# Performance work log

Measured on AMD Instinct MI355X. Metric: run time of the kernel, lower is better.

The kernel has to match this reference:

```python
import jax, jax.numpy as jnp
import numpy as np
from jax import lax

B, S, H = 1, 2048, 1024
NH, NKV, HD = 16, 4, 64        # heads, kv heads, head_dim = H // NH
I = 3584                        # intermediate size
E, TOPK = 8, 2                  # experts, top-k routing
EPS = 1e-5
THETA = 1e6


def setup_inputs() -> dict:
    key = jax.random.key(0)
    ks = jax.random.split(key, 12)
    sc = 0.02
    return {
        "hidden_states": jax.random.normal(ks[0], (B, S, H), jnp.float32),
        "position_ids": jnp.broadcast_to(jnp.arange(S, dtype=jnp.int32), (B, S)),
        "wq": jax.random.normal(ks[1], (H, NH * HD), jnp.float32) * sc,
        "wk": jax.random.normal(ks[2], (H, NKV * HD), jnp.float32) * sc,
        "wv": jax.random.normal(ks[3], (H, NKV * HD), jnp.float32) * sc,
        "wo": jax.random.normal(ks[4], (NH * HD, H), jnp.float32) * sc,
        "input_norm_w": jnp.ones((H,), jnp.float32),
        "post_norm_w": jnp.ones((H,), jnp.float32),
        "gate_w": jax.random.normal(ks[5], (H, E), jnp.float32) * sc,
        "w1": jax.random.normal(ks[6], (E, H, I), jnp.float32) * sc,
        "w3": jax.random.normal(ks[7], (E, H, I), jnp.float32) * sc,
        "w2": jax.random.normal(ks[8], (E, I, H), jnp.float32) * sc,
    }


def _rmsnorm(x, w):
    var = jnp.mean(jnp.square(x), axis=-1, keepdims=True)
    return x * lax.rsqrt(var + EPS) * w


def _rope(q, k, position_ids):
    # q: [B,S,NH,HD], k: [B,S,NKV,HD]
    inv_freq = 1.0 / (THETA ** (jnp.arange(0, HD, 2, dtype=jnp.float32) / HD))
    freqs = position_ids.astype(jnp.float32)[..., None] * inv_freq  # [B,S,HD/2]
    emb = jnp.concatenate([freqs, freqs], axis=-1)                  # [B,S,HD]
    cos = jnp.cos(emb)[:, :, None, :]
    sin = jnp.sin(emb)[:, :, None, :]

    def rot_half(x):
        x1, x2 = jnp.split(x, 2, axis=-1)
        return jnp.concatenate([-x2, x1], axis=-1)

    return q * cos + rot_half(q) * sin, k * cos + rot_half(k) * sin


def _attention(x, position_ids, wq, wk, wv, wo):
    b, s, _ = x.shape
    q = (x @ wq).reshape(b, s, NH, HD)
    k = (x @ wk).reshape(b, s, NKV, HD)
    v = (x @ wv).reshape(b, s, NKV, HD)
    q, k = _rope(q, k, position_ids)
    groups = NH // NKV
    k = jnp.repeat(k, groups, axis=2)  # [B,S,NH,HD]
    v = jnp.repeat(v, groups, axis=2)
    scale = HD ** -0.5
    scores = jnp.einsum("bqhd,bkhd->bhqk", q, k) * scale
    causal = jnp.tril(jnp.ones((s, s), dtype=bool))
    scores = jnp.where(causal[None, None], scores, jnp.finfo(scores.dtype).min)
    probs = jax.nn.softmax(scores, axis=-1)
    out = jnp.einsum("bhqk,bkhd->bqhd", probs, v).reshape(b, s, NH * HD)
    return out @ wo


def _moe(x, gate_w, w1, w3, w2):
    b, s, h = x.shape
    xt = x.reshape(b * s, h)
    logits = xt @ gate_w                      # [T,E]
    probs = jax.nn.softmax(logits, axis=-1)
    top_w, top_i = lax.top_k(probs, TOPK)     # [T,K]
    top_w = top_w / jnp.sum(top_w, axis=-1, keepdims=True)
    out = jnp.zeros_like(xt)
    for e in range(E):
        we = jnp.sum(jnp.where(top_i == e, top_w, 0.0), axis=-1)   # [T]
        h_e = jax.nn.silu(xt @ w1[e]) * (xt @ w3[e])               # [T,I]
        out = out + we[:, None] * (h_e @ w2[e])
    return out.reshape(b, s, h), logits


def reference(hidden_states, position_ids, wq, wk, wv, wo,
              input_norm_w, post_norm_w, gate_w, w1, w3, w2):
    # MixtralDecoderLayer: norm -> GQA attn -> residual -> norm -> MoE -> residual
    attn_out = _attention(_rmsnorm(hidden_states, input_norm_w),
                          position_ids, wq, wk, wv, wo)
    h = hidden_states + attn_out
    moe_out, _router_logits = _moe(_rmsnorm(h, post_norm_w), gate_w, w1, w3, w2)
    return h + moe_out
```

## Files before the change

kernel.cpp:

```cpp
#include <hip/hip_runtime.h>
#include <math.h>


typedef unsigned short u16;
typedef unsigned int u32;
typedef __attribute__((ext_vector_type(8))) short s16x8;
typedef __attribute__((ext_vector_type(8))) _Float16 f16x8;
typedef __attribute__((ext_vector_type(4))) float f32x4;

#define S_LEN 2048
#define HDIM  1024
#define NHEAD 16
#define NKVH  4
#define HD    64
#define ISZ   3584
#define NEXP  8
#define NSLOT 4096
#define EPS_F 1e-5f
#define NEG_INF -1e30f
#define LOG2E 1.44269504f

__device__ __forceinline__ float bf2f(u16 u) {
    union { u32 i; float f; } c; c.i = ((u32)u) << 16; return c.f;
}
__device__ __forceinline__ u16 f2bf(float f) {
    union { float f; u32 i; } c; c.f = f;
    u32 r = (c.i + 0x7fffu + ((c.i >> 16) & 1u)) >> 16;
    return (u16)r;
}
__device__ __forceinline__ u16 f2h_bits(float f) {
    union { _Float16 h; u16 u; } c; c.h = (_Float16)f; return c.u;
}
__device__ __forceinline__ void async16(const u16* g, u16* l) {
    __builtin_amdgcn_global_load_lds(
        (const __attribute__((address_space(1))) void*)g,
        (__attribute__((address_space(3))) void*)l, 16, 0, 0);
}

__global__ void k_zero_ints(int* __restrict__ p, int n) {
    int i = blockIdx.x * blockDim.x + threadIdx.x;
    if (i < n) p[i] = 0;
}

__global__ __launch_bounds__(256)
void k_rmsnorm_bf(const float* __restrict__ x, const float* __restrict__ w,
                  u16* __restrict__ out) {
    int t = blockIdx.x;
    int tid = threadIdx.x;
    float4 v = ((const float4*)(x + (size_t)t * HDIM))[tid];
    float ss = v.x * v.x + v.y * v.y + v.z * v.z + v.w * v.w;
#pragma unroll
    for (int off = 32; off >= 1; off >>= 1) ss += __shfl_xor(ss, off, 64);
    __shared__ float red[4];
    if ((tid & 63) == 0) red[tid >> 6] = ss;
    __syncthreads();
    float tot = red[0] + red[1] + red[2] + red[3];
    float rstd = rsqrtf(tot * (1.0f / HDIM) + EPS_F);
    float4 wv = ((const float4*)w)[tid];
    uint2 pk;
    pk.x = (u32)f2bf(v.x * rstd * wv.x) | ((u32)f2bf(v.y * rstd * wv.y) << 16);
    pk.y = (u32)f2bf(v.z * rstd * wv.z) | ((u32)f2bf(v.w * rstd * wv.w) << 16);
    ((uint2*)(out + (size_t)t * HDIM))[tid] = pk;
}

__global__ __launch_bounds__(256)
void k_cvt_t(const float* __restrict__ src, u16* __restrict__ dst,
             int R, int C, long long srcZ, long long dstZ) {
    const int z = blockIdx.z;
    src += (size_t)z * srcZ;
    dst += (size_t)z * dstZ;
    const int lane = threadIdx.x & 63, w = threadIdx.x >> 6;
    const int c = blockIdx.x * 64 + lane;
    const int r0 = blockIdx.y * 128 + w * 32;
    float v[32];
#pragma unroll
    for (int i = 0; i < 32; i++) v[i] = src[(size_t)(r0 + i) * C + c];
#pragma unroll
    for (int g = 0; g < 4; g++) {
        uint4 pk;
        pk.x = (u32)f2bf(v[g * 8 + 0]) | ((u32)f2bf(v[g * 8 + 1]) << 16);
        pk.y = (u32)f2bf(v[g * 8 + 2]) | ((u32)f2bf(v[g * 8 + 3]) << 16);
        pk.z = (u32)f2bf(v[g * 8 + 4]) | ((u32)f2bf(v[g * 8 + 5]) << 16);
        pk.w = (u32)f2bf(v[g * 8 + 6]) | ((u32)f2bf(v[g * 8 + 7]) << 16);
        *(uint4*)(&dst[(size_t)c * R + r0 + g * 8]) = pk;
    }
}

__device__ __forceinline__ void gemm128_loop(
    const u16* __restrict__ A, const u16* __restrict__ Bt, int K,
    int rowA0, int rowAmax, int n0, u16* lds, f32x4 acc[4][4]) {
    const int tid = threadIdx.x;
    const int lane = tid & 63, wid = tid >> 6;
    const int sr = lane >> 2, sc = lane & 3;
    const int ln = lane & 15, q = lane >> 4;
    const int wm = wid >> 1, wn = wid & 1;
    for (int k0 = 0; k0 < K; k0 += 32) {
        __syncthreads();
#pragma unroll
        for (int t = 0; t < 2; t++) {
            int row = wid * 32 + t * 16 + sr;
            int ck = (sc ^ (row & 3)) << 3;
            int ra = rowA0 + row;
            if (ra > rowAmax) ra = rowAmax;
            u16* ldsA = lds + (size_t)(wid * 32 + t * 16) * 32;
            u16* ldsB = ldsA + 4096;
            async16(A + (size_t)ra * K + k0 + ck, ldsA);
            async16(Bt + (size_t)(n0 + row) * K + k0 + ck, ldsB);
        }
        __syncthreads();
        s16x8 af[4], bfv[4];
#pragma unroll
        for (int i = 0; i < 4; i++) {
            int ar = wm * 64 + i * 16 + ln;
            af[i] = *(const s16x8*)(lds + ar * 32 + ((q ^ (ar & 3)) << 3));
            int br = wn * 64 + i * 16 + ln;
            bfv[i] = *(const s16x8*)(lds + 4096 + br * 32 + ((q ^ (br & 3)) << 3));
        }
#pragma unroll
        for (int i = 0; i < 4; i++)
#pragma unroll
            for (int j = 0; j < 4; j++)
                acc[i][j] = __builtin_amdgcn_mfma_f32_16x16x32_bf16(
                    af[i], bfv[j], acc[i][j], 0, 0, 0);
    }
}

__global__ __launch_bounds__(256, 2)
void k_gemm_bt(const u16* __restrict__ A, const u16* __restrict__ Bt,
               int M, int N, int K, int mode,
               float* __restrict__ F0, float* __restrict__ F1,
               const float* __restrict__ RES, u16* __restrict__ O16) {
    __shared__ u16 lds[8192];
    const int m0 = blockIdx.y * 128, n0 = blockIdx.x * 128;
    f32x4 acc[4][4];
#pragma unroll
    for (int i = 0; i < 4; i++)
#pragma unroll
        for (int j = 0; j < 4; j++) acc[i][j] = (f32x4){0.f, 0.f, 0.f, 0.f};
    gemm128_loop(A, Bt, K, m0, M - 1, n0, lds, acc);
    const int lane = threadIdx.x & 63, wid = threadIdx.x >> 6;
    const int ln = lane & 15, q = lane >> 4, wm = wid >> 1, wn = wid & 1;
#pragma unroll
    for (int i = 0; i < 4; i++) {
#pragma unroll
        for (int r = 0; r < 4; r++) {
            int m = m0 + wm * 64 + i * 16 + q * 4 + r;
#pragma unroll
            for (int j = 0; j < 4; j++) {
                int n = n0 + wn * 64 + j * 16 + ln;
                float v = acc[i][j][r];
                if (mode == 0) {
                    F0[(size_t)m * N + n] = v;
                } else if (mode == 1) {
                    O16[(size_t)m * N + n] = f2bf(v);
                } else if (mode == 2) {
                    F0[(size_t)m * N + n] = v + RES[(size_t)m * N + n];
                } else {
                    if (n < 1024)       F0[(size_t)m * 1024 + n] = v;
                    else if (n < 1280)  F1[(size_t)m * 256 + (n - 1024)] = v;
                    else                O16[(size_t)m * 256 + (n - 1280)] = f2h_bits(v);
                }
            }
        }
    }
}

__global__ __launch_bounds__(256, 2)
void k_gemm_bt_moe(const u16* __restrict__ A, const u16* __restrict__ WT,
                   int N, int K, int mode,
                   float* __restrict__ F0, u16* __restrict__ O16,
                   const u16* __restrict__ AUX, const int* __restrict__ offs) {
    const int e = blockIdx.z;
    const int base = offs[e], cnt = offs[e + 1] - base;
    const int m0 = blockIdx.y * 128;
    if (m0 >= cnt) return;
    __shared__ u16 lds[8192];
    const u16* Bt = WT + (size_t)e * N * K;
    const int n0 = blockIdx.x * 128;
    f32x4 acc[4][4];
#pragma unroll
    for (int i = 0; i < 4; i++)
#pragma unroll
        for (int j = 0; j < 4; j++) acc[i][j] = (f32x4){0.f, 0.f, 0.f, 0.f};
    gemm128_loop(A, WT + (size_t)e * N * K, K, base + m0, NSLOT - 1, n0, lds, acc);
    (void)Bt;
    const int lane = threadIdx.x & 63, wid = threadIdx.x >> 6;
    const int ln = lane & 15, q = lane >> 4, wm = wid >> 1, wn = wid & 1;
#pragma unroll
    for (int i = 0; i < 4; i++) {
#pragma unroll
        for (int r = 0; r < 4; r++) {
            int mloc = wm * 64 + i * 16 + q * 4 + r;
            if (m0 + mloc >= cnt) continue;
            size_t row = (size_t)(base + m0 + mloc);
#pragma unroll
            for (int j = 0; j < 4; j++) {
                int n = n0 + wn * 64 + j * 16 + ln;
                float v = acc[i][j][r];
                if (mode == 0) {
                    F0[row * N + n] = v;
                } else if (mode == 1) {
                    O16[row * N + n] = f2bf(v);
                } else {
                    float a = bf2f(AUX[row * N + n]);
                    float s = v / (1.0f + expf(-v));
                    O16[row * N + n] = f2bf(s * a);
                }
            }
        }
    }
}

__global__ __launch_bounds__(256)
void k_rope_cvt(const float* __restrict__ q, const float* __restrict__ k,
                const int* __restrict__ pos, u16* __restrict__ qb2,
                u16* __restrict__ kb2) {
    int id = blockIdx.x * blockDim.x + threadIdx.x;
    int d = id & 31;
    int hh = (id >> 5) % (NHEAD + NKVH);
    int s = id / ((NHEAD + NKVH) * 32);
    float p = (float)pos[s];
    float inv = exp2f(-((float)(2 * d) / (float)HD) * log2f(1.0e6f));
    float ang = p * inv;
    float c = cosf(ang), sn = sinf(ang);
    const float* sp; u16* dp;
    if (hh < NHEAD) {
        sp = q + (size_t)s * (NHEAD * HD) + hh * HD;
        dp = qb2 + (size_t)s * (NHEAD * HD) + hh * HD;
    } else {
        sp = k + (size_t)s * (NKVH * HD) + (hh - NHEAD) * HD;
        dp = kb2 + (size_t)s * (NKVH * HD) + (hh - NHEAD) * HD;
    }
    float x1 = sp[d], x2 = sp[d + 32];
    dp[d]      = f2h_bits(x1 * c - x2 * sn);
    dp[d + 32] = f2h_bits(x2 * c + x1 * sn);
}

__global__ __launch_bounds__(256)
void k_attn_mfma(const u16* __restrict__ qb, const u16* __restrict__ kb,
                 const u16* __restrict__ vb, u16* __restrict__ ob) {
    __shared__ u16 Qs[64 * 64];
    __shared__ u16 Ks[64 * 64];
    __shared__ u16 Vt[64 * 64];
    __shared__ u16 Ps[64 * 64];
    const int qt = blockIdx.x, h = blockIdx.y, kvh = h >> 2;
    const int tid = threadIdx.x, lane = tid & 63, w = tid >> 6;
    const int ln = lane & 15, quad = lane >> 4;

#pragma unroll
    for (int p = 0; p < 2; p++) {
        int r = p * 32 + (tid >> 3), c = tid & 7;
        uint4 v = *(const uint4*)(qb + (size_t)(qt * 64 + r) * (NHEAD * HD) +
                                  h * HD + c * 8);
        *(uint4*)&Qs[r * 64 + ((c ^ (r & 7)) << 3)] = v;
    }

    float m_[4], l_[4];
    f32x4 Oa[4];
#pragma unroll
    for (int r = 0; r < 4; r++) { m_[r] = NEG_INF; l_[r] = 0.0f; }
#pragma unroll
    for (int nt = 0; nt < 4; nt++) Oa[nt] = (f32x4){0.f, 0.f, 0.f, 0.f};

    for (int kt = 0; kt <= qt; kt++) {
        __syncthreads();
#pragma unroll
        for (int p = 0; p < 2; p++) {
            int r = p * 32 + (tid >> 3), c = tid & 7;
            uint4 v = *(const uint4*)(kb + (size_t)(kt * 64 + r) * (NKVH * HD) +
                                      kvh * HD + c * 8);
            *(uint4*)&Ks[r * 64 + ((c ^ (r & 7)) << 3)] = v;
        }
        {
            int s = tid & 63;
#pragma unroll
            for (int half = 0; half < 2; half++) {
                int d0 = w * 16 + half * 8;
                uint4 v = *(const uint4*)(vb + (size_t)(kt * 64 + s) * (NKVH * HD) +
                                          kvh * HD + d0);
                u16 a[8];
                a[0] = (u16)(v.x & 0xffff); a[1] = (u16)(v.x >> 16);
                a[2] = (u16)(v.y & 0xffff); a[3] = (u16)(v.y >> 16);
                a[4] = (u16)(v.z & 0xffff); a[5] = (u16)(v.z >> 16);
                a[6] = (u16)(v.w & 0xffff); a[7] = (u16)(v.w >> 16);
#pragma unroll
                for (int j = 0; j < 8; j++) {
                    int d = d0 + j;
                    Vt[d * 64 + (((s >> 3) ^ (d & 7)) << 3) + (s & 7)] = a[j];
                }
            }
        }
        __syncthreads();

        f32x4 sc[4];
#pragma unroll
        for (int nt = 0; nt < 4; nt++) sc[nt] = (f32x4){0.f, 0.f, 0.f, 0.f};
#pragma unroll
        for (int ks = 0; ks < 2; ks++) {
            int arow = 16 * w + ln;
            f16x8 af = *(const f16x8*)&Qs[arow * 64 +
                                          (((ks * 4 + quad) ^ (arow & 7)) << 3)];
#pragma unroll
            for (int nt = 0; nt < 4; nt++) {
                int brow = nt * 16 + ln;
                f16x8 bf = *(const f16x8*)&Ks[brow * 64 +
                                              (((ks * 4 + quad) ^ (brow & 7)) << 3)];
                sc[nt] = __builtin_amdgcn_mfma_f32_16x16x32_f16(af, bf, sc[nt],
                                                                0, 0, 0);
            }
        }

        const bool diag = (kt == qt);
        float mt[4];
#pragma unroll
        for (int r = 0; r < 4; r++) {
            int qrow = quad * 4 + r + 16 * w;
#pragma unroll
            for (int nt = 0; nt < 4; nt++) {
                float s = sc[nt][r] * 0.125f;
                if (diag && (nt * 16 + ln) > qrow) s = NEG_INF;
                sc[nt][r] = s;
            }
            mt[r] = fmaxf(fmaxf(sc[0][r], sc[1][r]), fmaxf(sc[2][r], sc[3][r]));
        }
#pragma unroll
        for (int off = 8; off >= 1; off >>= 1)
#pragma unroll
            for (int r = 0; r < 4; r++)
                mt[r] = fmaxf(mt[r], __shfl_xor(mt[r], off, 64));

        float rs[4];
#pragma unroll
        for (int r = 0; r < 4; r++) {
            float mn = fmaxf(m_[r], mt[r]);
            float al = exp2f((m_[r] - mn) * LOG2E);
            m_[r] = mn;
            float acc0 = 0.0f;
#pragma unroll
            for (int nt = 0; nt < 4; nt++) {
                float pv = exp2f((sc[nt][r] - mn) * LOG2E);
                sc[nt][r] = pv;
                acc0 += pv;
            }
            rs[r] = acc0;
            l_[r] *= al;
#pragma unroll
            for (int nt = 0; nt < 4; nt++) Oa[nt][r] *= al;
        }
#pragma unroll
        for (int off = 8; off >= 1; off >>= 1)
#pragma unroll
            for (int r = 0; r < 4; r++) rs[r] += __shfl_xor(rs[r], off, 64);
#pragma unroll
        for (int r = 0; r < 4; r++) l_[r] += rs[r];

#pragma unroll
        for (int r = 0; r < 4; r++) {
            int row = 16 * w + quad * 4 + r;
#pragma unroll
            for (int nt = 0; nt < 4; nt++) {
                int ch = nt * 2 + (ln >> 3);
                Ps[row * 64 + ((ch ^ (row & 7)) << 3) + (ln & 7)] =
                    f2h_bits(sc[nt][r]);
            }
        }
        __syncthreads();

#pragma unroll
        for (int ks = 0; ks < 2; ks++) {
            int arow = 16 * w + ln;
            f16x8 pf = *(const f16x8*)&Ps[arow * 64 +
                                          (((ks * 4 + quad) ^ (arow & 7)) << 3)];
#pragma unroll
            for (int nt = 0; nt < 4; nt++) {
                int vrow = nt * 16 + ln;
                f16x8 vf = *(const f16x8*)&Vt[vrow * 64 +
                                              (((ks * 4 + quad) ^ (vrow & 7)) << 3)];
                Oa[nt] = __builtin_amdgcn_mfma_f32_16x16x32_f16(pf, vf, Oa[nt],
                                                                0, 0, 0);
            }
        }
    }

#pragma unroll
    for (int r = 0; r < 4; r++) {
        float inv = 1.0f / l_[r];
        int sg = qt * 64 + 16 * w + quad * 4 + r;
#pragma unroll
        for (int nt = 0; nt < 4; nt++) {
            int d = nt * 16 + ln;
            ob[(size_t)sg * HDIM + h * HD + d] = f2bf(Oa[nt][r] * inv);
        }
    }
}

__global__ __launch_bounds__(64)
void k_gate(const float* __restrict__ Hst, const float* __restrict__ PW,
            const float* __restrict__ GW, int* __restrict__ cnt,
            int* __restrict__ top_i, float* __restrict__ top_w) {
    int t = blockIdx.x;
    int lane = threadIdx.x;
    const float* hrow = Hst + (size_t)t * HDIM;
    float ss = 0.0f;
    float acc[NEXP] = {};
    for (int hh = lane; hh < HDIM; hh += 64) {
        float hv = hrow[hh];
        ss += hv * hv;
        float xw = hv * PW[hh];
        const float* g = GW + (size_t)hh * NEXP;
#pragma unroll
        for (int e = 0; e < NEXP; e++) acc[e] += xw * g[e];
    }
#pragma unroll
    for (int off = 32; off >= 1; off >>= 1) {
        ss += __shfl_xor(ss, off, 64);
#pragma unroll
        for (int e = 0; e < NEXP; e++) acc[e] += __shfl_xor(acc[e], off, 64);
    }
    if (lane == 0) {
        float rstd = rsqrtf(ss * (1.0f / HDIM) + EPS_F);
        int e0 = 0;
        for (int e = 1; e < NEXP; e++) if (acc[e] > acc[e0]) e0 = e;
        int e1 = (e0 == 0) ? 1 : 0;
        for (int e = 0; e < NEXP; e++)
            if (e != e0 && acc[e] > acc[e1]) e1 = e;
        float w0 = 1.0f / (1.0f + expf((acc[e1] - acc[e0]) * rstd));
        top_i[t * 2 + 0] = e0; top_i[t * 2 + 1] = e1;
        top_w[t * 2 + 0] = w0; top_w[t * 2 + 1] = 1.0f - w0;
        atomicAdd(&cnt[e0], 1);
        atomicAdd(&cnt[e1], 1);
    }
}

__global__ void k_prefix(const int* __restrict__ cnt, int* __restrict__ offs,
                         int* __restrict__ cur) {
    if (blockIdx.x == 0 && threadIdx.x == 0) {
        int a = 0;
        for (int e = 0; e < NEXP; e++) { offs[e] = a; cur[e] = a; a += cnt[e]; }
        offs[NEXP] = a;
    }
}

__global__ __launch_bounds__(256)
void k_fill(const int* __restrict__ top_i, int* __restrict__ cur,
            int* __restrict__ idxg, int* __restrict__ slot) {
    int t = blockIdx.x * blockDim.x + threadIdx.x;
    if (t >= S_LEN) return;
#pragma unroll
    for (int kk = 0; kk < 2; kk++) {
        int e = top_i[t * 2 + kk];
        int p = atomicAdd(&cur[e], 1);
        idxg[p] = t;
        slot[t * 2 + kk] = p;
    }
}

__global__ __launch_bounds__(256)
void k_gather(const u16* __restrict__ xnb, const int* __restrict__ idxg,
              u16* __restrict__ Xg) {
    int p = blockIdx.x;
    int t = idxg[p];
    const uint2* s = (const uint2*)(xnb + (size_t)t * HDIM);
    uint2* d = (uint2*)(Xg + (size_t)p * HDIM);
    d[threadIdx.x] = s[threadIdx.x];
}

__global__ __launch_bounds__(256)
void k_combine(const float* __restrict__ oexp, const int* __restrict__ slot,
               const float* __restrict__ top_w, float* __restrict__ out) {
    int t = blockIdx.x, tid = threadIdx.x;
    int s0 = slot[t * 2], s1 = slot[t * 2 + 1];
    float w0 = top_w[t * 2], w1 = top_w[t * 2 + 1];
    float4 a = ((const float4*)(oexp + (size_t)s0 * HDIM))[tid];
    float4 b = ((const float4*)(oexp + (size_t)s1 * HDIM))[tid];
    float4* o = (float4*)(out + (size_t)t * HDIM);
    float4 c = o[tid];
    c.x += w0 * a.x + w1 * b.x;
    c.y += w0 * a.y + w1 * b.y;
    c.z += w0 * a.z + w1 * b.z;
    c.w += w0 * a.w + w1 * b.w;
    o[tid] = c;
}

extern "C" void kernel_launch(void* const* d_in, const int* in_sizes, int n_in,
                              void* d_out, int out_size, void* d_ws,
                              size_t ws_size, hipStream_t stream) {
    (void)in_sizes; (void)n_in; (void)out_size; (void)ws_size;
    const float* hidden = (const float*)d_in[0];
    const int*   pos    = (const int*)d_in[1];
    const float* wq     = (const float*)d_in[2];
    const float* wk     = (const float*)d_in[3];
    const float* wv     = (const float*)d_in[4];
    const float* wo     = (const float*)d_in[5];
    const float* innw   = (const float*)d_in[6];
    const float* postnw = (const float*)d_in[7];
    const float* gatew  = (const float*)d_in[8];
    const float* w1     = (const float*)d_in[9];
    const float* w3     = (const float*)d_in[10];
    const float* w2     = (const float*)d_in[11];
    float* out = (float*)d_out;

    u16* w1t  = (u16*)d_ws;
    u16* w3t  = w1t + (size_t)NEXP * ISZ * HDIM;
    u16* w2t  = w3t + (size_t)NEXP * ISZ * HDIM;
    u16* qkvt = w2t + (size_t)NEXP * ISZ * HDIM;
    u16* wot  = qkvt + (size_t)1536 * HDIM;
    u16* xnb  = wot + (size_t)HDIM * HDIM;
    float* qbuf = (float*)(xnb + (size_t)S_LEN * HDIM);
    float* kbuf = qbuf + (size_t)S_LEN * HDIM;
    u16* vb16   = (u16*)(kbuf + (size_t)S_LEN * NKVH * HD);
    u16* qb2    = vb16 + (size_t)S_LEN * NKVH * HD;
    u16* kb2    = qb2 + (size_t)S_LEN * HDIM;
    u16* attnb  = kb2 + (size_t)S_LEN * NKVH * HD;
    float* oexp = qbuf;
    u16* Xg  = attnb + (size_t)S_LEN * HDIM;
    u16* hg3 = Xg + (size_t)NSLOT * HDIM;
    u16* he  = hg3 + (size_t)NSLOT * ISZ;
    int* ib  = (int*)(he + (size_t)NSLOT * ISZ);
    int*   cnt   = ib;
    int*   offs  = ib + 16;
    int*   cur   = ib + 32;
    int*   top_i = ib + 64;
    int*   slot  = ib + 64 + 4096;
    int*   idxg  = ib + 64 + 8192;
    float* top_w = (float*)(ib + 64 + 12288);

    const long long HI = (long long)HDIM * ISZ;

    k_zero_ints<<<1, 64, 0, stream>>>(cnt, 64);
    k_rmsnorm_bf<<<S_LEN, 256, 0, stream>>>(hidden, innw, xnb);

    k_cvt_t<<<dim3(16, 8, 1), 256, 0, stream>>>(wq, qkvt, 1024, 1024, 0, 0);
    k_cvt_t<<<dim3(4, 8, 1), 256, 0, stream>>>(wk, qkvt + (size_t)1024 * 1024, 1024, 256, 0, 0);
    k_cvt_t<<<dim3(4, 8, 1), 256, 0, stream>>>(wv, qkvt + (size_t)1280 * 1024, 1024, 256, 0, 0);
    k_cvt_t<<<dim3(16, 8, 1), 256, 0, stream>>>(wo, wot, 1024, 1024, 0, 0);
    k_cvt_t<<<dim3(56, 8, NEXP), 256, 0, stream>>>(w1, w1t, 1024, 3584, HI, HI);
    k_cvt_t<<<dim3(56, 8, NEXP), 256, 0, stream>>>(w3, w3t, 1024, 3584, HI, HI);
    k_cvt_t<<<dim3(16, 28, NEXP), 256, 0, stream>>>(w2, w2t, 3584, 1024, HI, HI);

    k_gemm_bt<<<dim3(12, 16), 256, 0, stream>>>(xnb, qkvt, 2048, 1536, 1024, 3,
                                                qbuf, kbuf, nullptr, vb16);
    k_rope_cvt<<<(S_LEN * (NHEAD + NKVH) * 32) / 256, 256, 0, stream>>>(
        qbuf, kbuf, pos, qb2, kb2);
    k_attn_mfma<<<dim3(32, 16), 256, 0, stream>>>(qb2, kb2, vb16, attnb);
    k_gemm_bt<<<dim3(8, 16), 256, 0, stream>>>(attnb, wot, 2048, 1024, 1024, 2,
                                               out, nullptr, hidden, nullptr);
    k_rmsnorm_bf<<<S_LEN, 256, 0, stream>>>(out, postnw, xnb);
    k_gate<<<S_LEN, 64, 0, stream>>>(out, postnw, gatew, cnt, top_i, top_w);
    k_prefix<<<1, 1, 0, stream>>>(cnt, offs, cur);
    k_fill<<<S_LEN / 256, 256, 0, stream>>>(top_i, cur, idxg, slot);
    k_gather<<<NSLOT, 256, 0, stream>>>(xnb, idxg, Xg);

    k_gemm_bt_moe<<<dim3(28, 16, NEXP), 256, 0, stream>>>(Xg, w3t, 3584, 1024, 1,
                                                          nullptr, hg3, nullptr, offs);
    k_gemm_bt_moe<<<dim3(28, 16, NEXP), 256, 0, stream>>>(Xg, w1t, 3584, 1024, 2,
                                                          nullptr, he, hg3, offs);
    k_gemm_bt_moe<<<dim3(8, 16, NEXP), 256, 0, stream>>>(he, w2t, 1024, 3584, 0,
                                                         oexp, nullptr, nullptr, offs);
    k_combine<<<S_LEN, 256, 0, stream>>>(oexp, slot, top_w, out);
}
```

Baseline: 1.000 ms.

## Double-buffer GEMM LDS staging and split-K the MoE down projection

The shared GEMM main loop now uses two LDS buffers, issuing async loads for the next 32-wide K slice before computing on the current one. This removes one barrier per iteration and lets global loads overlap with MFMA work. The MoE w2 GEMM is also split into two K halves written to separate fp32 buffers, doubling the grid for the long-K launch, and the combine kernel sums both halves. The cost is twice the LDS per block, which may lower occupancy, plus an extra fp32 intermediate buffer and more memory traffic in the combine step.

```diff
diff --git a/kernel.cpp b/kernel.cpp
--- a/kernel.cpp
+++ b/kernel.cpp
@@ -86,35 +86,47 @@
     }
 }
 
-__device__ __forceinline__ void gemm128_loop(
+__device__ __forceinline__ void stage32(const u16* __restrict__ A,
+                                        const u16* __restrict__ Bt, int K,
+                                        int rowA0, int rowAmax, int n0, int kc,
+                                        u16* buf, int wid, int sr, int sc) {
+#pragma unroll
+    for (int t = 0; t < 2; t++) {
+        int row = wid * 32 + t * 16 + sr;
+        int ck = (sc ^ (row & 3)) << 3;
+        int ra = rowA0 + row;
+        if (ra > rowAmax) ra = rowAmax;
+        u16* ldsA = buf + (wid * 32 + t * 16) * 32;
+        async16(A + (size_t)ra * K + kc + ck, ldsA);
+        async16(Bt + (size_t)(n0 + row) * K + kc + ck, ldsA + 4096);
+    }
+}
+
+__device__ __forceinline__ void gemm128_dbuf(
     const u16* __restrict__ A, const u16* __restrict__ Bt, int K,
-    int rowA0, int rowAmax, int n0, u16* lds, f32x4 acc[4][4]) {
+    int kbeg, int kend, int rowA0, int rowAmax, int n0,
+    u16* lds, f32x4 acc[4][4]) {
     const int tid = threadIdx.x;
     const int lane = tid & 63, wid = tid >> 6;
     const int sr = lane >> 2, sc = lane & 3;
     const int ln = lane & 15, q = lane >> 4;
     const int wm = wid >> 1, wn = wid & 1;
-    for (int k0 = 0; k0 < K; k0 += 32) {
+    stage32(A, Bt, K, rowA0, rowAmax, n0, kbeg, lds, wid, sr, sc);
+    int pp = 0;
+    for (int kc = kbeg; kc < kend; kc += 32) {
+        u16* cur = lds + pp * 8192;
+        u16* nxt = lds + (pp ^ 1) * 8192;
+        pp ^= 1;
         __syncthreads();
-#pragma unroll
-        for (int t = 0; t < 2; t++) {
-            int row = wid * 32 + t * 16 + sr;
-            int ck = (sc ^ (row & 3)) << 3;
-            int ra = rowA0 + row;
-            if (ra > rowAmax) ra = rowAmax;
-            u16* ldsA = lds + (size_t)(wid * 32 + t * 16) * 32;
-            u16* ldsB = ldsA + 4096;
-            async16(A + (size_t)ra * K + k0 + ck, ldsA);
-            async16(Bt + (size_t)(n0 + row) * K + k0 + ck, ldsB);
-        }
-        __syncthreads();
+        if (kc + 32 < kend)
+            stage32(A, Bt, K, rowA0, rowAmax, n0, kc + 32, nxt, wid, sr, sc);
         s16x8 af[4], bfv[4];
 #pragma unroll
         for (int i = 0; i < 4; i++) {
             int ar = wm * 64 + i * 16 + ln;
-            af[i] = *(const s16x8*)(lds + ar * 32 + ((q ^ (ar & 3)) << 3));
+            af[i] = *(const s16x8*)(cur + ar * 32 + ((q ^ (ar & 3)) << 3));
             int br = wn * 64 + i * 16 + ln;
-            bfv[i] = *(const s16x8*)(lds + 4096 + br * 32 + ((q ^ (br & 3)) << 3));
+            bfv[i] = *(const s16x8*)(cur + 4096 + br * 32 + ((q ^ (br & 3)) << 3));
         }
 #pragma unroll
         for (int i = 0; i < 4; i++)
@@ -130,14 +142,14 @@
                int M, int N, int K, int mode,
                float* __restrict__ F0, float* __restrict__ F1,
                const float* __restrict__ RES, u16* __restrict__ O16) {
-    __shared__ u16 lds[8192];
+    __shared__ u16 lds[16384];
     const int m0 = blockIdx.y * 128, n0 = blockIdx.x * 128;
     f32x4 acc[4][4];
 #pragma unroll
     for (int i = 0; i < 4; i++)
 #pragma unroll
         for (int j = 0; j < 4; j++) acc[i][j] = (f32x4){0.f, 0.f, 0.f, 0.f};
-    gemm128_loop(A, Bt, K, m0, M - 1, n0, lds, acc);
+    gemm128_dbuf(A, Bt, K, 0, K, m0, M - 1, n0, lds, acc);
     const int lane = threadIdx.x & 63, wid = threadIdx.x >> 6;
     const int ln = lane & 15, q = lane >> 4, wm = wid >> 1, wn = wid & 1;
 #pragma unroll
@@ -168,13 +180,13 @@
 __global__ __launch_bounds__(256, 2)
 void k_gemm_bt_moe(const u16* __restrict__ A, const u16* __restrict__ WT,
                    int N, int K, int mode,
-                   float* __restrict__ F0, u16* __restrict__ O16,
-                   const u16* __restrict__ AUX, const int* __restrict__ offs) {
+                   u16* __restrict__ O16, const u16* __restrict__ AUX,
+                   const int* __restrict__ offs) {
     const int e = blockIdx.z;
     const int base = offs[e], cnt = offs[e + 1] - base;
     const int m0 = blockIdx.y * 128;
     if (m0 >= cnt) return;
-    __shared__ u16 lds[8192];
+    __shared__ u16 lds[16384];
     const u16* Bt = WT + (size_t)e * N * K;
     const int n0 = blockIdx.x * 128;
     f32x4 acc[4][4];
@@ -182,8 +194,7 @@
     for (int i = 0; i < 4; i++)
 #pragma unroll
         for (int j = 0; j < 4; j++) acc[i][j] = (f32x4){0.f, 0.f, 0.f, 0.f};
-    gemm128_loop(A, WT + (size_t)e * N * K, K, base + m0, NSLOT - 1, n0, lds, acc);
-    (void)Bt;
+    gemm128_dbuf(A, Bt, K, 0, K, base + m0, NSLOT - 1, n0, lds, acc);
     const int lane = threadIdx.x & 63, wid = threadIdx.x >> 6;
     const int ln = lane & 15, q = lane >> 4, wm = wid >> 1, wn = wid & 1;
 #pragma unroll
@@ -197,15 +208,51 @@
             for (int j = 0; j < 4; j++) {
                 int n = n0 + wn * 64 + j * 16 + ln;
                 float v = acc[i][j][r];
-                if (mode == 0) {
-                    F0[row * N + n] = v;
-                } else if (mode == 1) {
+                if (mode == 1) {
                     O16[row * N + n] = f2bf(v);
                 } else {
                     float a = bf2f(AUX[row * N + n]);
                     float s = v / (1.0f + expf(-v));
                     O16[row * N + n] = f2bf(s * a);
                 }
+            }
+        }
+    }
+}
+
+__global__ __launch_bounds__(256, 2)
+void k_moe_w2(const u16* __restrict__ He, const u16* __restrict__ W2T,
+              float* __restrict__ OA, float* __restrict__ OB,
+              const int* __restrict__ offs) {
+    const int z = blockIdx.z;
+    const int e = z & 7, half = z >> 3;
+    const int base = offs[e], cnt = offs[e + 1] - base;
+    const int m0 = blockIdx.y * 128;
+    if (m0 >= cnt) return;
+    __shared__ u16 lds[16384];
+    const u16* Bt = W2T + (size_t)e * HDIM * ISZ;
+    const int n0 = blockIdx.x * 128;
+    f32x4 acc[4][4];
+#pragma unroll
+    for (int i = 0; i < 4; i++)
+#pragma unroll
+        for (int j = 0; j < 4; j++) acc[i][j] = (f32x4){0.f, 0.f, 0.f, 0.f};
+    gemm128_dbuf(He, Bt, ISZ, half * (ISZ / 2), (half + 1) * (ISZ / 2),
+                 base + m0, NSLOT - 1, n0, lds, acc);
+    float* F0 = half ? OB : OA;
+    const int lane = threadIdx.x & 63, wid = threadIdx.x >> 6;
+    const int ln = lane & 15, q = lane >> 4, wm = wid >> 1, wn = wid & 1;
+#pragma unroll
+    for (int i = 0; i < 4; i++) {
+#pragma unroll
+        for (int r = 0; r < 4; r++) {
+            int mloc = wm * 64 + i * 16 + q * 4 + r;
+            if (m0 + mloc >= cnt) continue;
+            size_t row = (size_t)(base + m0 + mloc);
+#pragma unroll
+            for (int j = 0; j < 4; j++) {
+                int n = n0 + wn * 64 + j * 16 + ln;
+                F0[row * HDIM + n] = acc[i][j][r];
             }
         }
     }
@@ -466,19 +513,22 @@
 }
 
 __global__ __launch_bounds__(256)
-void k_combine(const float* __restrict__ oexp, const int* __restrict__ slot,
-               const float* __restrict__ top_w, float* __restrict__ out) {
+void k_combine2(const float* __restrict__ OA, const float* __restrict__ OB,
+                const int* __restrict__ slot, const float* __restrict__ top_w,
+                float* __restrict__ out) {
     int t = blockIdx.x, tid = threadIdx.x;
     int s0 = slot[t * 2], s1 = slot[t * 2 + 1];
     float w0 = top_w[t * 2], w1 = top_w[t * 2 + 1];
-    float4 a = ((const float4*)(oexp + (size_t)s0 * HDIM))[tid];
-    float4 b = ((const float4*)(oexp + (size_t)s1 * HDIM))[tid];
+    float4 a0 = ((const float4*)(OA + (size_t)s0 * HDIM))[tid];
+    float4 b0 = ((const float4*)(OB + (size_t)s0 * HDIM))[tid];
+    float4 a1 = ((const float4*)(OA + (size_t)s1 * HDIM))[tid];
+    float4 b1 = ((const float4*)(OB + (size_t)s1 * HDIM))[tid];
     float4* o = (float4*)(out + (size_t)t * HDIM);
     float4 c = o[tid];
-    c.x += w0 * a.x + w1 * b.x;
-    c.y += w0 * a.y + w1 * b.y;
-    c.z += w0 * a.z + w1 * b.z;
-    c.w += w0 * a.w + w1 * b.w;
+    c.x += w0 * (a0.x + b0.x) + w1 * (a1.x + b1.x);
+    c.y += w0 * (a0.y + b0.y) + w1 * (a1.y + b1.y);
+    c.z += w0 * (a0.z + b0.z) + w1 * (a1.z + b1.z);
+    c.w += w0 * (a0.w + b0.w) + w1 * (a1.w + b1.w);
     o[tid] = c;
 }
 
@@ -512,11 +562,12 @@
     u16* qb2    = vb16 + (size_t)S_LEN * NKVH * HD;
     u16* kb2    = qb2 + (size_t)S_LEN * HDIM;
     u16* attnb  = kb2 + (size_t)S_LEN * NKVH * HD;
-    float* oexp = qbuf;
+    float* oexpA = qbuf;
     u16* Xg  = attnb + (size_t)S_LEN * HDIM;
     u16* hg3 = Xg + (size_t)NSLOT * HDIM;
     u16* he  = hg3 + (size_t)NSLOT * ISZ;
-    int* ib  = (int*)(he + (size_t)NSLOT * ISZ);
+    float* oexpB = (float*)(he + (size_t)NSLOT * ISZ);
+    int* ib  = (int*)(oexpB + (size_t)NSLOT * HDIM);
     int*   cnt   = ib;
     int*   offs  = ib + 16;
     int*   cur   = ib + 32;
@@ -552,10 +603,9 @@
     k_gather<<<NSLOT, 256, 0, stream>>>(xnb, idxg, Xg);
 
     k_gemm_bt_moe<<<dim3(28, 16, NEXP), 256, 0, stream>>>(Xg, w3t, 3584, 1024, 1,
-                                                          nullptr, hg3, nullptr, offs);
+                                                          hg3, nullptr, offs);
     k_gemm_bt_moe<<<dim3(28, 16, NEXP), 256, 0, stream>>>(Xg, w1t, 3584, 1024, 2,
-                                                          nullptr, he, hg3, offs);
-    k_gemm_bt_moe<<<dim3(8, 16, NEXP), 256, 0, stream>>>(he, w2t, 1024, 3584, 0,
-                                                         oexp, nullptr, nullptr, offs);
-    k_combine<<<S_LEN, 256, 0, stream>>>(oexp, slot, top_w, out);
-}
+                                                          he, hg3, offs);
+    k_moe_w2<<<dim3(8, 16, 16), 256, 0, stream>>>(he, w2t, oexpA, oexpB, offs);
+    k_combine2<<<S_LEN, 256, 0, stream>>>(oexpA, oexpB, slot, top_w, out);
+}
```

After: 924.5 us. 7.6% less time.
